# Kernel tuning notes

Measured on AMD Instinct MI355X. Metric: run time of the kernel, lower is better.

The kernel has to match this reference:

```python
import jax, jax.numpy as jnp
import numpy as np


def setup_inputs() -> dict:
    key = jax.random.key(0)
    k1, k2, k3, k4, k5, k6 = jax.random.split(key, 6)
    B, N, K = 2, 60000, 16
    C_in, C_add, C_mid = 64, 3, 16
    out_features = 128
    in_features = (C_in + C_add) * C_mid  # 1072
    return {
        "input_features": jax.random.normal(k1, (B, N, C_in), dtype=jnp.float32),
        "neighbor_inds": jax.random.randint(k2, (B, N, K), 0, N, dtype=jnp.int32),
        "weightnet": jax.random.normal(k3, (B, N, K, C_mid), dtype=jnp.float32),
        "additional_features": jax.random.normal(k4, (B, N, K, C_add), dtype=jnp.float32),
        "linear_weight": jax.random.normal(k5, (out_features, in_features), dtype=jnp.float32) * 0.03,
        "linear_bias": jax.random.normal(k6, (out_features,), dtype=jnp.float32),
    }


def reference(input_features, neighbor_inds, weightnet, additional_features, linear_weight, linear_bias):
    # Gather neighbor features: [B, N, K, C_in]
    gathered = jax.vmap(lambda feats, idx: feats[idx])(input_features, neighbor_inds)
    # Concat per-neighbor additional features: [B, N, K, C_in + C_add]
    feat = jnp.concatenate([gathered, additional_features], axis=-1)
    # PConv: contract over neighbors K against weightnet -> [B, N, C, M]
    pconv = jnp.einsum('bnkc,bnkm->bncm', feat, weightnet)
    B, N = pconv.shape[0], pconv.shape[1]
    pconv = pconv.reshape(B, N, -1)  # [B, N, (C_in+C_add)*C_mid]
    # Fused linear projection
    return jnp.einsum('bnf,of->bno', pconv, linear_weight) + linear_bias
```

## Files before the change

kernel.cpp:

```cpp
#include <hip/hip_runtime.h>

#define NPTS  60000
#define NBLK  1875
#define FP    1088
#define PSTR  1096
#define SPBYTES (32 * PSTR * 2)
#define LWH_BYTES   (128 * FP * 2)
#define INF16_BYTES (2 * NPTS * 64 * 2)
#define WS_NEED     (LWH_BYTES + INF16_BYTES)

typedef _Float16 f16x4 __attribute__((ext_vector_type(4)));
typedef _Float16 f16x8 __attribute__((ext_vector_type(8)));
typedef float    f32x4 __attribute__((ext_vector_type(4)));

__global__ void __launch_bounds__(256)
cvt_lw_kernel(const float* __restrict__ LW, _Float16* __restrict__ LWh) {
    const int o = blockIdx.x;
    for (int f = threadIdx.x; f < FP; f += 256) {
        const float v = (f < 1072) ? LW[o * 1072 + f] : 0.f;
        LWh[(f >> 5) * (128 * 32) + o * 32 + (f & 31)] = (_Float16)v;
    }
}

__global__ void __launch_bounds__(256)
cvt_inf_kernel(const float* __restrict__ inF, _Float16* __restrict__ inF16) {
    const int tid = blockIdx.x * 256 + threadIdx.x;
    if (tid >= 2 * NPTS * 64) return;
    const int c = tid & 63;
    const int n = tid >> 6;
    inF16[(n << 6) + ((c & 15) << 2) + (c >> 4)] = (_Float16)inF[tid];
}

template<bool F16P> struct GRegs;
template<> struct GRegs<true>  { f16x4 fv[4];    float wv[4]; float av[4]; };
template<> struct GRegs<false> { float fv[4][4]; float wv[4]; float av[4]; };

static __device__ __forceinline__ void issue_gather16(
    const _Float16* __restrict__ inF16, const float* __restrict__ Wn,
    const float* __restrict__ addF, int bbase, int base_nk,
    int ind_lane, int i, int q, int ml, bool mlo, GRegs<true>& g)
{
    #pragma unroll
    for (int j = 0; j < 4; ++j) {
        const int k   = q * 4 + j;
        const int idx = __shfl(ind_lane, i * 16 + k, 64);
        g.fv[j] = *(const f16x4*)(inF16 + (bbase + idx) * 64 + ml * 4);
        g.wv[j] = Wn[(base_nk + k) * 16 + ml];
        g.av[j] = mlo ? addF[(base_nk + k) * 3 + ml] : 0.f;
    }
}

static __device__ __forceinline__ void issue_gather32(
    const float* __restrict__ inF, const float* __restrict__ Wn,
    const float* __restrict__ addF, int bbase, int base_nk,
    int ind_lane, int i, int q, int ml, bool mlo, GRegs<false>& g)
{
    #pragma unroll
    for (int j = 0; j < 4; ++j) {
        const int k   = q * 4 + j;
        const int idx = __shfl(ind_lane, i * 16 + k, 64);
        const float* fp = inF + (bbase + idx) * 64 + ml;
        #pragma unroll
        for (int ct = 0; ct < 4; ++ct)
            g.fv[ct][j] = fp[ct * 16];
        g.wv[j] = Wn[(base_nk + k) * 16 + ml];
        g.av[j] = mlo ? addF[(base_nk + k) * 3 + ml] : 0.f;
    }
}

template<bool F16P>
static __device__ __forceinline__ void compute_point(
    const GRegs<F16P>& g, _Float16* sProw, int qsw, int ml, bool mlo)
{
    const f32x4 z4 = {0.f, 0.f, 0.f, 0.f};
    f16x4 aW, bA;
    #pragma unroll
    for (int j = 0; j < 4; ++j) { aW[j] = (_Float16)g.wv[j]; bA[j] = (_Float16)g.av[j]; }

    #pragma unroll
    for (int ct = 0; ct < 4; ++ct) {
        f16x4 bF;
        #pragma unroll
        for (int j = 0; j < 4; ++j) {
            if constexpr (F16P) bF[j] = g.fv[j][ct];
            else                bF[j] = (_Float16)g.fv[ct][j];
        }
        const f32x4 d = __builtin_amdgcn_mfma_f32_16x16x16f16(aW, bF, z4, 0, 0, 0);
        f16x4 dh;
        #pragma unroll
        for (int r = 0; r < 4; ++r) dh[r] = (_Float16)d[r];
        *(f16x4*)&sProw[(ct * 16 + ml) * 16 + qsw * 4] = dh;
    }
    const f32x4 d = __builtin_amdgcn_mfma_f32_16x16x16f16(aW, bA, z4, 0, 0, 0);
    if (mlo) {
        f16x4 dh;
        #pragma unroll
        for (int r = 0; r < 4; ++r) dh[r] = (_Float16)d[r];
        *(f16x4*)&sProw[(64 + ml) * 16 + qsw * 4] = dh;
    }
}

template<bool F16P>
__global__ void __launch_bounds__(512, 4)
pconv_linear_mfma(const float* __restrict__ inF,
                  const _Float16* __restrict__ inF16,
                  const int*   __restrict__ inds,
                  const float* __restrict__ Wn,
                  const float* __restrict__ addF,
                  const _Float16* __restrict__ LWh,
                  const float* __restrict__ bias,
                  float*       __restrict__ out)
{
    extern __shared__ __align__(16) _Float16 sP[];

    const int t    = threadIdx.x;
    const int lane = t & 63;
    const int w    = t >> 6;
    const int q    = lane >> 4;
    const int ml   = lane & 15;
    const bool mlo = (ml < 3);
    const int qsw  = q ^ (((ml >> 2) & 1) << 1);

    const int bid   = blockIdx.x;
    const int b     = bid / NBLK;
    const int n0    = (bid - b * NBLK) * 32;
    const int bbase = b * NPTS;

    const int ind_lane = inds[(bbase + n0 + w * 4) * 16 + lane];

    sP[(t >> 4) * PSTR + 1072 + (t & 15)] = (_Float16)0.f;

    const int nk0 = (bbase + n0 + w * 4) * 16;
    _Float16* sPw = sP + (w * 4) * PSTR;
    if constexpr (F16P) {
        GRegs<true> g0, g1, g2, g3;
        issue_gather16(inF16, Wn, addF, bbase, nk0,      ind_lane, 0, q, ml, mlo, g0);
        issue_gather16(inF16, Wn, addF, bbase, nk0 + 16, ind_lane, 1, q, ml, mlo, g1);
        issue_gather16(inF16, Wn, addF, bbase, nk0 + 32, ind_lane, 2, q, ml, mlo, g2);
        issue_gather16(inF16, Wn, addF, bbase, nk0 + 48, ind_lane, 3, q, ml, mlo, g3);
        compute_point<true>(g0, sPw,            qsw, ml, mlo);
        compute_point<true>(g1, sPw + PSTR,     qsw, ml, mlo);
        compute_point<true>(g2, sPw + 2 * PSTR, qsw, ml, mlo);
        compute_point<true>(g3, sPw + 3 * PSTR, qsw, ml, mlo);
    } else {
        GRegs<false> g0, g1;
        issue_gather32(inF, Wn, addF, bbase, nk0,      ind_lane, 0, q, ml, mlo, g0);
        issue_gather32(inF, Wn, addF, bbase, nk0 + 16, ind_lane, 1, q, ml, mlo, g1);
        compute_point<false>(g0, sPw,            qsw, ml, mlo);
        issue_gather32(inF, Wn, addF, bbase, nk0 + 32, ind_lane, 2, q, ml, mlo, g0);
        compute_point<false>(g1, sPw + PSTR,     qsw, ml, mlo);
        issue_gather32(inF, Wn, addF, bbase, nk0 + 48, ind_lane, 3, q, ml, mlo, g1);
        compute_point<false>(g0, sPw + 2 * PSTR, qsw, ml, mlo);
        compute_point<false>(g1, sPw + 3 * PSTR, qsw, ml, mlo);
    }

    const int o0 = w * 16;
    const _Float16* bP = LWh + (o0 + ml) * 32 + q * 8;
    f16x8 bcur = *(const f16x8*)(bP);
    f16x8 bnxt = *(const f16x8*)(bP + 4096);
    __syncthreads();

    const float bz = bias[o0 + ml];
    f32x4 acc0 = {0.f, 0.f, 0.f, 0.f};
    f32x4 acc1 = {0.f, 0.f, 0.f, 0.f};
    const _Float16* aP0 = sP + ml * PSTR + (q >> 1) * 16 + (q & 1) * 8;
    const _Float16* aP1 = aP0 + 16 * PSTR;
    const int flip = (q & 1) ? -8 : 8;

    #pragma unroll 2
    for (int ch = 0; ch < 34; ++ch) {
        const int chf = (ch + 2 < 34) ? (ch + 2) : 33;
        f16x8 bfut = *(const f16x8*)(bP + chf * 4096);
        const int off = ch * 32 + ((ch & 2) ? flip : 0);
        f16x8 a0 = *(const f16x8*)(aP0 + off);
        f16x8 a1 = *(const f16x8*)(aP1 + off);
        acc0 = __builtin_amdgcn_mfma_f32_16x16x32_f16(a0, bcur, acc0, 0, 0, 0);
        acc1 = __builtin_amdgcn_mfma_f32_16x16x32_f16(a1, bcur, acc1, 0, 0, 0);
        bcur = bnxt; bnxt = bfut;
    }

    float* ob = out + (bbase + n0 + q * 4) * 128 + o0 + ml;
    #pragma unroll
    for (int r = 0; r < 4; ++r)
        ob[r * 128] = acc0[r] + bz;
    ob += 16 * 128;
    #pragma unroll
    for (int r = 0; r < 4; ++r)
        ob[r * 128] = acc1[r] + bz;
}

extern "C" void kernel_launch(void* const* d_in, const int* in_sizes, int n_in,
                              void* d_out, int out_size, void* d_ws, size_t ws_size,
                              hipStream_t stream)
{
    const float* inF  = (const float*)d_in[0];
    const int*   inds = (const int*)  d_in[1];
    const float* Wn   = (const float*)d_in[2];
    const float* addF = (const float*)d_in[3];
    const float* LW   = (const float*)d_in[4];
    const float* bias = (const float*)d_in[5];
    float* out = (float*)d_out;
    _Float16* LWh = (_Float16*)d_ws;

    const bool f16p = (ws_size >= (size_t)WS_NEED);

    hipFuncSetAttribute((const void*)pconv_linear_mfma<true>,
                        hipFuncAttributeMaxDynamicSharedMemorySize, SPBYTES);
    hipFuncSetAttribute((const void*)pconv_linear_mfma<false>,
                        hipFuncAttributeMaxDynamicSharedMemorySize, SPBYTES);

    cvt_lw_kernel<<<dim3(128), dim3(256), 0, stream>>>(LW, LWh);
    if (f16p) {
        _Float16* inF16 = (_Float16*)((char*)d_ws + LWH_BYTES);
        cvt_inf_kernel<<<dim3((2 * NPTS * 64 + 255) / 256), dim3(256), 0, stream>>>(
            inF, inF16);
        pconv_linear_mfma<true><<<dim3(2 * NBLK), dim3(512), SPBYTES, stream>>>(
            inF, inF16, inds, Wn, addF, LWh, bias, out);
    } else {
        pconv_linear_mfma<false><<<dim3(2 * NBLK), dim3(512), SPBYTES, stream>>>(
            inF, (const _Float16*)nullptr, inds, Wn, addF, LWh, bias, out);
    }
}
```

Baseline: 362.4 us.

## Make fp16 path a persistent kernel with register-resident weights and gather prefetch

Replaces the one-tile-per-block launch with 250 persistent blocks that each process 15 tiles. The linear weight fragments are loaded into registers once per block and reused for every tile. The next tile's gathers are issued while the current tile is computed, and the LDS staging is double-buffered so only one barrier per tile is needed. This trades occupancy (launch bounds drop to 2 blocks per CU, with heavy register pressure from the 34 weight fragments) for removing the per-tile weight reloads and hiding gather latency. The 250 blocks may also under-fill the GPU's CUs.

```diff
diff --git a/kernel.cpp b/kernel.cpp
--- a/kernel.cpp
+++ b/kernel.cpp
@@ -4,10 +4,14 @@
 #define NBLK  1875
 #define FP    1088
 #define PSTR  1096
-#define SPBYTES (32 * PSTR * 2)
+#define HALF  (32 * PSTR)
+#define SPBYTES    (2 * HALF * 2)
+#define SPBYTES_FB (32 * PSTR * 2)
 #define LWH_BYTES   (128 * FP * 2)
 #define INF16_BYTES (2 * NPTS * 64 * 2)
 #define WS_NEED     (LWH_BYTES + INF16_BYTES)
+#define TILES   15
+#define NBLOCKS 250
 
 typedef _Float16 f16x4 __attribute__((ext_vector_type(4)));
 typedef _Float16 f16x8 __attribute__((ext_vector_type(8)));
@@ -31,14 +35,11 @@
     inF16[(n << 6) + ((c & 15) << 2) + (c >> 4)] = (_Float16)inF[tid];
 }
 
-template<bool F16P> struct GRegs;
-template<> struct GRegs<true>  { f16x4 fv[4];    float wv[4]; float av[4]; };
-template<> struct GRegs<false> { float fv[4][4]; float wv[4]; float av[4]; };
+struct GR { f16x4 fv[4]; float wv[4]; };
 
 static __device__ __forceinline__ void issue_gather16(
     const _Float16* __restrict__ inF16, const float* __restrict__ Wn,
-    const float* __restrict__ addF, int bbase, int base_nk,
-    int ind_lane, int i, int q, int ml, bool mlo, GRegs<true>& g)
+    int bbase, int base_nk, int ind_lane, int i, int q, int ml, GR& g)
 {
     #pragma unroll
     for (int j = 0; j < 4; ++j) {
@@ -46,51 +47,37 @@
         const int idx = __shfl(ind_lane, i * 16 + k, 64);
         g.fv[j] = *(const f16x4*)(inF16 + (bbase + idx) * 64 + ml * 4);
         g.wv[j] = Wn[(base_nk + k) * 16 + ml];
-        g.av[j] = mlo ? addF[(base_nk + k) * 3 + ml] : 0.f;
-    }
-}
-
-static __device__ __forceinline__ void issue_gather32(
-    const float* __restrict__ inF, const float* __restrict__ Wn,
-    const float* __restrict__ addF, int bbase, int base_nk,
-    int ind_lane, int i, int q, int ml, bool mlo, GRegs<false>& g)
-{
-    #pragma unroll
-    for (int j = 0; j < 4; ++j) {
-        const int k   = q * 4 + j;
-        const int idx = __shfl(ind_lane, i * 16 + k, 64);
-        const float* fp = inF + (bbase + idx) * 64 + ml;
-        #pragma unroll
-        for (int ct = 0; ct < 4; ++ct)
-            g.fv[ct][j] = fp[ct * 16];
-        g.wv[j] = Wn[(base_nk + k) * 16 + ml];
-        g.av[j] = mlo ? addF[(base_nk + k) * 3 + ml] : 0.f;
-    }
-}
-
-template<bool F16P>
+    }
+}
+
 static __device__ __forceinline__ void compute_point(
-    const GRegs<F16P>& g, _Float16* sProw, int qsw, int ml, bool mlo)
-{
+    const GR& g, const float* __restrict__ aFp,
+    _Float16* sProw, int qsw, int q, int ml, bool mlo)
+{
+    float av[4];
+    #pragma unroll
+    for (int j = 0; j < 4; ++j)
+        av[j] = mlo ? aFp[(q * 4 + j) * 3] : 0.f;
+
     const f32x4 z4 = {0.f, 0.f, 0.f, 0.f};
-    f16x4 aW, bA;
-    #pragma unroll
-    for (int j = 0; j < 4; ++j) { aW[j] = (_Float16)g.wv[j]; bA[j] = (_Float16)g.av[j]; }
+    f16x4 aW;
+    #pragma unroll
+    for (int j = 0; j < 4; ++j) aW[j] = (_Float16)g.wv[j];
 
     #pragma unroll
     for (int ct = 0; ct < 4; ++ct) {
         f16x4 bF;
         #pragma unroll
-        for (int j = 0; j < 4; ++j) {
-            if constexpr (F16P) bF[j] = g.fv[j][ct];
-            else                bF[j] = (_Float16)g.fv[ct][j];
-        }
+        for (int j = 0; j < 4; ++j) bF[j] = g.fv[j][ct];
         const f32x4 d = __builtin_amdgcn_mfma_f32_16x16x16f16(aW, bF, z4, 0, 0, 0);
         f16x4 dh;
         #pragma unroll
         for (int r = 0; r < 4; ++r) dh[r] = (_Float16)d[r];
         *(f16x4*)&sProw[(ct * 16 + ml) * 16 + qsw * 4] = dh;
     }
+    f16x4 bA;
+    #pragma unroll
+    for (int j = 0; j < 4; ++j) bA[j] = (_Float16)av[j];
     const f32x4 d = __builtin_amdgcn_mfma_f32_16x16x16f16(aW, bA, z4, 0, 0, 0);
     if (mlo) {
         f16x4 dh;
@@ -100,16 +87,14 @@
     }
 }
 
-template<bool F16P>
-__global__ void __launch_bounds__(512, 4)
-pconv_linear_mfma(const float* __restrict__ inF,
-                  const _Float16* __restrict__ inF16,
-                  const int*   __restrict__ inds,
-                  const float* __restrict__ Wn,
-                  const float* __restrict__ addF,
-                  const _Float16* __restrict__ LWh,
-                  const float* __restrict__ bias,
-                  float*       __restrict__ out)
+__global__ void __launch_bounds__(512, 2)
+pconv_persistent(const _Float16* __restrict__ inF16,
+                 const int*   __restrict__ inds,
+                 const float* __restrict__ Wn,
+                 const float* __restrict__ addF,
+                 const _Float16* __restrict__ LWh,
+                 const float* __restrict__ bias,
+                 float*       __restrict__ out)
 {
     extern __shared__ __align__(16) _Float16 sP[];
 
@@ -121,38 +106,162 @@
     const bool mlo = (ml < 3);
     const int qsw  = q ^ (((ml >> 2) & 1) << 1);
 
-    const int bid   = blockIdx.x;
-    const int b     = bid / NBLK;
-    const int n0    = (bid - b * NBLK) * 32;
-    const int bbase = b * NPTS;
-
+    sP[(t >> 4) * PSTR + 1072 + (t & 15)] = (_Float16)0.f;
+    sP[HALF + (t >> 4) * PSTR + 1072 + (t & 15)] = (_Float16)0.f;
+
+    const int o0 = w * 16;
+    const _Float16* bPw = LWh + (o0 + ml) * 32 + q * 8;
+    f16x8 bfr[34];
+    #pragma unroll
+    for (int ch = 0; ch < 34; ++ch)
+        bfr[ch] = *(const f16x8*)(bPw + ch * 4096);
+    const float bz = bias[o0 + ml];
+
+    int gt  = blockIdx.x * TILES;
+    int bC  = gt / NBLK;
+    int n0C = (gt - bC * NBLK) * 32;
+    int bbC = bC * NPTS;
+    int nkC = (bbC + n0C + w * 4) * 16;
+    GR g0, g1, g2, g3;
+    {
+        const int ind0 = inds[nkC + lane];
+        issue_gather16(inF16, Wn, bbC, nkC,      ind0, 0, q, ml, g0);
+        issue_gather16(inF16, Wn, bbC, nkC + 16, ind0, 1, q, ml, g1);
+        issue_gather16(inF16, Wn, bbC, nkC + 32, ind0, 2, q, ml, g2);
+        issue_gather16(inF16, Wn, bbC, nkC + 48, ind0, 3, q, ml, g3);
+    }
+
+    for (int tt = 0; tt < TILES; ++tt) {
+        const bool more = (tt + 1 < TILES);
+        int bbN = bbC, n0N = n0C, nkN = nkC, indN = 0;
+        if (more) {
+            const int gtn = gt + 1;
+            const int bN  = gtn / NBLK;
+            n0N = (gtn - bN * NBLK) * 32;
+            bbN = bN * NPTS;
+            nkN = (bbN + n0N + w * 4) * 16;
+            indN = inds[nkN + lane];
+        }
+
+        _Float16* sPc = sP + (tt & 1) * HALF;
+        _Float16* sPw = sPc + (w * 4) * PSTR;
+        const float* aFp = addF + nkC * 3 + ml;
+
+        compute_point(g0, aFp,       sPw,            qsw, q, ml, mlo);
+        compute_point(g1, aFp + 48,  sPw + PSTR,     qsw, q, ml, mlo);
+        if (more) {
+            issue_gather16(inF16, Wn, bbN, nkN,      indN, 0, q, ml, g0);
+            issue_gather16(inF16, Wn, bbN, nkN + 16, indN, 1, q, ml, g1);
+        }
+        compute_point(g2, aFp + 96,  sPw + 2 * PSTR, qsw, q, ml, mlo);
+        compute_point(g3, aFp + 144, sPw + 3 * PSTR, qsw, q, ml, mlo);
+        if (more) {
+            issue_gather16(inF16, Wn, bbN, nkN + 32, indN, 2, q, ml, g2);
+            issue_gather16(inF16, Wn, bbN, nkN + 48, indN, 3, q, ml, g3);
+        }
+        __syncthreads();
+
+        f32x4 acc0 = {0.f, 0.f, 0.f, 0.f};
+        f32x4 acc1 = {0.f, 0.f, 0.f, 0.f};
+        const _Float16* aP0 = sPc + ml * PSTR + (q >> 1) * 16 + (q & 1) * 8;
+        const _Float16* aP1 = aP0 + 16 * PSTR;
+        const int flip = (q & 1) ? -8 : 8;
+        #pragma unroll
+        for (int ch = 0; ch < 34; ++ch) {
+            const int off = ch * 32 + ((ch & 2) ? flip : 0);
+            f16x8 a0 = *(const f16x8*)(aP0 + off);
+            f16x8 a1 = *(const f16x8*)(aP1 + off);
+            acc0 = __builtin_amdgcn_mfma_f32_16x16x32_f16(a0, bfr[ch], acc0, 0, 0, 0);
+            acc1 = __builtin_amdgcn_mfma_f32_16x16x32_f16(a1, bfr[ch], acc1, 0, 0, 0);
+        }
+
+        float* ob = out + (bbC + n0C + q * 4) * 128 + o0 + ml;
+        #pragma unroll
+        for (int r = 0; r < 4; ++r)
+            ob[r * 128] = acc0[r] + bz;
+        ob += 16 * 128;
+        #pragma unroll
+        for (int r = 0; r < 4; ++r)
+            ob[r * 128] = acc1[r] + bz;
+
+        bbC = bbN; n0C = n0N; nkC = nkN; ++gt;
+    }
+}
+
+struct GR32 { float fv[4][4]; float wv[4]; float av[4]; };
+
+static __device__ __forceinline__ void issue_gather32(
+    const float* __restrict__ inF, const float* __restrict__ Wn,
+    const float* __restrict__ addF, int bbase, int base_nk,
+    int ind_lane, int i, int q, int ml, bool mlo, GR32& g)
+{
+    #pragma unroll
+    for (int j = 0; j < 4; ++j) {
+        const int k   = q * 4 + j;
+        const int idx = __shfl(ind_lane, i * 16 + k, 64);
+        const float* fp = inF + (bbase + idx) * 64 + ml;
+        #pragma unroll
+        for (int ct = 0; ct < 4; ++ct)
+            g.fv[ct][j] = fp[ct * 16];
+        g.wv[j] = Wn[(base_nk + k) * 16 + ml];
+        g.av[j] = mlo ? addF[(base_nk + k) * 3 + ml] : 0.f;
+    }
+}
+
+static __device__ __forceinline__ void compute_point32(
+    const GR32& g, _Float16* sProw, int qsw, int ml, bool mlo)
+{
+    const f32x4 z4 = {0.f, 0.f, 0.f, 0.f};
+    f16x4 aW, bA;
+    #pragma unroll
+    for (int j = 0; j < 4; ++j) { aW[j] = (_Float16)g.wv[j]; bA[j] = (_Float16)g.av[j]; }
+    #pragma unroll
+    for (int ct = 0; ct < 4; ++ct) {
+        f16x4 bF;
+        #pragma unroll
+        for (int j = 0; j < 4; ++j) bF[j] = (_Float16)g.fv[ct][j];
+        const f32x4 d = __builtin_amdgcn_mfma_f32_16x16x16f16(aW, bF, z4, 0, 0, 0);
+        f16x4 dh;
+        #pragma unroll
+        for (int r = 0; r < 4; ++r) dh[r] = (_Float16)d[r];
+        *(f16x4*)&sProw[(ct * 16 + ml) * 16 + qsw * 4] = dh;
+    }
+    const f32x4 d = __builtin_amdgcn_mfma_f32_16x16x16f16(aW, bA, z4, 0, 0, 0);
+    if (mlo) {
+        f16x4 dh;
+        #pragma unroll
+        for (int r = 0; r < 4; ++r) dh[r] = (_Float16)d[r];
+        *(f16x4*)&sProw[(64 + ml) * 16 + qsw * 4] = dh;
+    }
+}
+
+__global__ void __launch_bounds__(512, 4)
+pconv_fallback(const float* __restrict__ inF, const int* __restrict__ inds,
+               const float* __restrict__ Wn, const float* __restrict__ addF,
+               const _Float16* __restrict__ LWh, const float* __restrict__ bias,
+               float* __restrict__ out)
+{
+    extern __shared__ __align__(16) _Float16 sP[];
+    const int t = threadIdx.x, lane = t & 63, w = t >> 6;
+    const int q = lane >> 4, ml = lane & 15;
+    const bool mlo = (ml < 3);
+    const int qsw = q ^ (((ml >> 2) & 1) << 1);
+    const int bid = blockIdx.x, b = bid / NBLK;
+    const int n0 = (bid - b * NBLK) * 32, bbase = b * NPTS;
     const int ind_lane = inds[(bbase + n0 + w * 4) * 16 + lane];
-
     sP[(t >> 4) * PSTR + 1072 + (t & 15)] = (_Float16)0.f;
 
     const int nk0 = (bbase + n0 + w * 4) * 16;
     _Float16* sPw = sP + (w * 4) * PSTR;
-    if constexpr (F16P) {
-        GRegs<true> g0, g1, g2, g3;
-        issue_gather16(inF16, Wn, addF, bbase, nk0,      ind_lane, 0, q, ml, mlo, g0);
-        issue_gather16(inF16, Wn, addF, bbase, nk0 + 16, ind_lane, 1, q, ml, mlo, g1);
-        issue_gather16(inF16, Wn, addF, bbase, nk0 + 32, ind_lane, 2, q, ml, mlo, g2);
-        issue_gather16(inF16, Wn, addF, bbase, nk0 + 48, ind_lane, 3, q, ml, mlo, g3);
-        compute_point<true>(g0, sPw,            qsw, ml, mlo);
-        compute_point<true>(g1, sPw + PSTR,     qsw, ml, mlo);
-        compute_point<true>(g2, sPw + 2 * PSTR, qsw, ml, mlo);
-        compute_point<true>(g3, sPw + 3 * PSTR, qsw, ml, mlo);
-    } else {
-        GRegs<false> g0, g1;
-        issue_gather32(inF, Wn, addF, bbase, nk0,      ind_lane, 0, q, ml, mlo, g0);
-        issue_gather32(inF, Wn, addF, bbase, nk0 + 16, ind_lane, 1, q, ml, mlo, g1);
-        compute_point<false>(g0, sPw,            qsw, ml, mlo);
-        issue_gather32(inF, Wn, addF, bbase, nk0 + 32, ind_lane, 2, q, ml, mlo, g0);
-        compute_point<false>(g1, sPw + PSTR,     qsw, ml, mlo);
-        issue_gather32(inF, Wn, addF, bbase, nk0 + 48, ind_lane, 3, q, ml, mlo, g1);
-        compute_point<false>(g0, sPw + 2 * PSTR, qsw, ml, mlo);
-        compute_point<false>(g1, sPw + 3 * PSTR, qsw, ml, mlo);
-    }
+    GR32 g0, g1;
+    issue_gather32(inF, Wn, addF, bbase, nk0,      ind_lane, 0, q, ml, mlo, g0);
+    issue_gather32(inF, Wn, addF, bbase, nk0 + 16, ind_lane, 1, q, ml, mlo, g1);
+    compute_point32(g0, sPw,            qsw, ml, mlo);
+    issue_gather32(inF, Wn, addF, bbase, nk0 + 32, ind_lane, 2, q, ml, mlo, g0);
+    compute_point32(g1, sPw + PSTR,     qsw, ml, mlo);
+    issue_gather32(inF, Wn, addF, bbase, nk0 + 48, ind_lane, 3, q, ml, mlo, g1);
+    compute_point32(g0, sPw + 2 * PSTR, qsw, ml, mlo);
+    compute_point32(g1, sPw + 3 * PSTR, qsw, ml, mlo);
 
     const int o0 = w * 16;
     const _Float16* bP = LWh + (o0 + ml) * 32 + q * 8;
@@ -166,7 +275,6 @@
     const _Float16* aP0 = sP + ml * PSTR + (q >> 1) * 16 + (q & 1) * 8;
     const _Float16* aP1 = aP0 + 16 * PSTR;
     const int flip = (q & 1) ? -8 : 8;
-
     #pragma unroll 2
     for (int ch = 0; ch < 34; ++ch) {
         const int chf = (ch + 2 < 34) ? (ch + 2) : 33;
@@ -178,15 +286,12 @@
         acc1 = __builtin_amdgcn_mfma_f32_16x16x32_f16(a1, bcur, acc1, 0, 0, 0);
         bcur = bnxt; bnxt = bfut;
     }
-
     float* ob = out + (bbase + n0 + q * 4) * 128 + o0 + ml;
     #pragma unroll
-    for (int r = 0; r < 4; ++r)
-        ob[r * 128] = acc0[r] + bz;
+    for (int r = 0; r < 4; ++r) ob[r * 128] = acc0[r] + bz;
     ob += 16 * 128;
     #pragma unroll
-    for (int r = 0; r < 4; ++r)
-        ob[r * 128] = acc1[r] + bz;
+    for (int r = 0; r < 4; ++r) ob[r * 128] = acc1[r] + bz;
 }
 
 extern "C" void kernel_launch(void* const* d_in, const int* in_sizes, int n_in,
@@ -204,20 +309,20 @@
 
     const bool f16p = (ws_size >= (size_t)WS_NEED);
 
-    hipFuncSetAttribute((const void*)pconv_linear_mfma<true>,
+    hipFuncSetAttribute((const void*)pconv_persistent,
                         hipFuncAttributeMaxDynamicSharedMemorySize, SPBYTES);
-    hipFuncSetAttribute((const void*)pconv_linear_mfma<false>,
-                        hipFuncAttributeMaxDynamicSharedMemorySize, SPBYTES);
+    hipFuncSetAttribute((const void*)pconv_fallback,
+                        hipFuncAttributeMaxDynamicSharedMemorySize, SPBYTES_FB);
 
     cvt_lw_kernel<<<dim3(128), dim3(256), 0, stream>>>(LW, LWh);
     if (f16p) {
         _Float16* inF16 = (_Float16*)((char*)d_ws + LWH_BYTES);
         cvt_inf_kernel<<<dim3((2 * NPTS * 64 + 255) / 256), dim3(256), 0, stream>>>(
             inF, inF16);
-        pconv_linear_mfma<true><<<dim3(2 * NBLK), dim3(512), SPBYTES, stream>>>(
-            inF, inF16, inds, Wn, addF, LWh, bias, out);
+        pconv_persistent<<<dim3(NBLOCKS), dim3(512), SPBYTES, stream>>>(
+            inF16, inds, Wn, addF, LWh, bias, out);
     } else {
-        pconv_linear_mfma<false><<<dim3(2 * NBLK), dim3(512), SPBYTES, stream>>>(
-            inF, (const _Float16*)nullptr, inds, Wn, addF, LWh, bias, out);
-    }
-}
+        pconv_fallback<<<dim3(2 * NBLK), dim3(512), SPBYTES_FB, stream>>>(
+            inF, inds, Wn, addF, LWh, bias, out);
+    }
+}
```

New measurement: 330.8 us. 1.1x faster.
